# Optimization experiments

Measured on AMD Instinct MI355X. Metric: run time of the kernel, lower is better.

Reference implementation:

```python
import jax, jax.numpy as jnp
import numpy as np

HID, NL, DSTATE, DCONV, EXPAND = 256, 2, 64, 4, 2
DIN = EXPAND * HID            # 512
NHEADS = DIN // 64            # 8 heads, headdim 64
HEADP = DIN // NHEADS         # 64
CONVDIM = DIN + 2 * DSTATE    # 640
PROJDIM = 2 * DIN + 2 * DSTATE + NHEADS  # 1160
B, T, NB = 2, 192, 62


def _rmsnorm(x, w, eps=1e-6):
    return x * jax.lax.rsqrt(jnp.mean(x * x, -1, keepdims=True) + eps) * w


def _causal_conv(x, w, b):
    # x (B,L,C), depthwise causal conv, w (C,K), b (C,)
    K = w.shape[1]
    L = x.shape[1]
    xp = jnp.pad(x, ((0, 0), (K - 1, 0), (0, 0)))
    y = b
    for k in range(K):
        y = y + xp[:, k:k + L, :] * w[:, k]
    return y


def _ssd(xh, dt, A, Bm, Cm):
    # quadratic (attention-like) form of the Mamba2 selective scan
    # xh (b,l,h,p), dt (b,l,h), A (h,), Bm/Cm (b,l,n)
    cum = jnp.cumsum(dt * A, axis=1)                    # (b,l,h)
    diff = cum[:, :, None, :] - cum[:, None, :, :]      # (b,l,s,h), <=0 for s<=l
    mask = jnp.tril(jnp.ones((xh.shape[1], xh.shape[1]), bool))
    decay = jnp.where(mask[None, :, :, None], jnp.exp(diff), 0.0)
    scores = jnp.einsum('bln,bsn->bls', Cm, Bm)[..., None] * decay * dt[:, None, :, :]
    return jnp.einsum('blsh,bshp->blhp', scores, xh)


def _mamba2(x, Win, Wconv, bconv, dt_bias, A_log, D, gn_w, Wout):
    b, l, _ = x.shape
    zxbcdt = x @ Win                                    # (b,l,PROJDIM)
    z = zxbcdt[..., :DIN]
    xBC = jax.nn.silu(_causal_conv(zxbcdt[..., DIN:DIN + CONVDIM], Wconv, bconv))
    xh = xBC[..., :DIN].reshape(b, l, NHEADS, HEADP)
    Bm = xBC[..., DIN:DIN + DSTATE]
    Cm = xBC[..., DIN + DSTATE:]
    dt = jax.nn.softplus(zxbcdt[..., -NHEADS:] + dt_bias)
    A = -jnp.exp(A_log)
    rev = lambda t: t[:, ::-1]
    y = _ssd(xh, dt, A, Bm, Cm) + rev(_ssd(rev(xh), rev(dt), A, rev(Bm), rev(Cm)))
    y = y + D[None, None, :, None] * xh
    y = _rmsnorm(y.reshape(b, l, DIN) * jax.nn.silu(z), gn_w)
    return y @ Wout


def _forward(x, tp, bp):
    batch, T_, NB_, H_ = x.shape
    for i in range(NL):
        # time axis: sequences of length T over batch*num_bands
        xt = jnp.transpose(x, (0, 2, 1, 3)).reshape(batch * NB_, T_, H_)
        xt = xt + _mamba2(_rmsnorm(xt, tp[0][i]), *(p[i] for p in tp[1:]))
        x = jnp.transpose(xt.reshape(batch, NB_, T_, H_), (0, 2, 1, 3))
        # band axis: sequences of length NB over batch*time
        xb = x.reshape(batch * T_, NB_, H_)
        xb = xb + _mamba2(_rmsnorm(xb, bp[0][i]), *(p[i] for p in bp[1:]))
        x = xb.reshape(batch, T_, NB_, H_)
    return x


def setup_inputs() -> dict:
    key = jax.random.key(0)
    ks = jax.random.split(key, 3)
    inp = {"x": jax.random.normal(ks[0], (B, T, NB, HID), jnp.float32)}
    for i, ax in enumerate(("t", "b")):
        kk = jax.random.split(ks[1 + i], 5)
        inp[ax + "_norm_w"] = jnp.ones((NL, HID), jnp.float32)
        inp[ax + "_Win"] = jax.random.normal(kk[0], (NL, HID, PROJDIM), jnp.float32) * HID ** -0.5
        inp[ax + "_Wconv"] = jax.random.normal(kk[1], (NL, CONVDIM, DCONV), jnp.float32) * DCONV ** -0.5
        inp[ax + "_bconv"] = jnp.zeros((NL, CONVDIM), jnp.float32)
        dt = jnp.exp(jax.random.uniform(kk[2], (NL, NHEADS)) * (np.log(0.1) - np.log(0.001)) + np.log(0.001))
        inp[ax + "_dt_bias"] = jnp.log(jnp.expm1(dt)).astype(jnp.float32)
        inp[ax + "_A_log"] = jnp.log(jax.random.uniform(kk[3], (NL, NHEADS), minval=1.0, maxval=16.0)).astype(jnp.float32)
        inp[ax + "_D"] = jnp.ones((NL, NHEADS), jnp.float32)
        inp[ax + "_gn_w"] = jnp.ones((NL, DIN), jnp.float32)
        inp[ax + "_Wout"] = jax.random.normal(kk[4], (NL, DIN, HID), jnp.float32) * DIN ** -0.5
    return inp


def reference(x, t_norm_w, t_Win, t_Wconv, t_bconv, t_dt_bias, t_A_log, t_D, t_gn_w, t_Wout,
              b_norm_w, b_Win, b_Wconv, b_bconv, b_dt_bias, b_A_log, b_D, b_gn_w, b_Wout):
    tp = (t_norm_w, t_Win, t_Wconv, t_bconv, t_dt_bias, t_A_log, t_D, t_gn_w, t_Wout)
    bp = (b_norm_w, b_Win, b_Wconv, b_bconv, b_dt_bias, b_A_log, b_D, b_gn_w, b_Wout)
    return _forward(x, tp, bp)
```

## Files before the change

kernel.cpp:

```cpp
#include <hip/hip_runtime.h>
#include <hip/hip_bf16.h>


#define MTOK   23808
#define PROJP  1280
#define ZXW    1152

typedef __attribute__((ext_vector_type(8))) short short8v;
typedef __attribute__((ext_vector_type(4))) short short4v;
typedef __attribute__((ext_vector_type(4))) float f32x4;

__device__ __forceinline__ float wave_sum64(float v) {
#pragma unroll
  for (int off = 32; off; off >>= 1) v += __shfl_xor(v, off, 64);
  return v;
}

__device__ __forceinline__ short f2bf(float f) {
  union { float f; unsigned u; } v; v.f = f;
  unsigned r = (v.u + 0x7fffu + ((v.u >> 16) & 1u)) >> 16;
  return (short)r;
}
__device__ __forceinline__ float bf2f(short s) {
  union { unsigned u; float f; } v; v.u = ((unsigned)(unsigned short)s) << 16; return v.f;
}

__device__ __forceinline__ long t_base(int m) {
  int seq = m / 192, tt = m - seq * 192;
  int b = seq / 62, nb = seq - b * 62;
  return ((long)((b * 192 + tt) * 62 + nb)) * 256;
}

__global__ __launch_bounds__(256) void k_wt(const float* __restrict__ tW,
                                            const float* __restrict__ bW,
                                            short* __restrict__ dst, int K, int N, int NP) {
  int z = blockIdx.z;
  const float* src = (z >> 1 ? bW : tW) + (long)(z & 1) * K * N;
  short* d = dst + (long)z * NP * K;
  int idx = blockIdx.x * 256 + threadIdx.x;
  if (idx >= NP * K) return;
  int n = idx / K, k = idx - n * K;
  d[idx] = (n < N) ? f2bf(src[(long)k * N + n]) : (short)0;
}

template <bool TPATH>
__global__ __launch_bounds__(256) void k_rmsnorm_in(const float* __restrict__ xio,
                                                    const float* __restrict__ w,
                                                    short* __restrict__ outb) {
  int m = blockIdx.x * 4 + (threadIdx.x >> 6);
  int lane = threadIdx.x & 63;
  long base = TPATH ? t_base(m) : (long)m * 256;
  float4 v = *(const float4*)(xio + base + lane * 4);
  float ss = v.x * v.x + v.y * v.y + v.z * v.z + v.w * v.w;
  ss = wave_sum64(ss);
  float sc = rsqrtf(ss * (1.f / 256.f) + 1e-6f);
  float4 wv = *(const float4*)(w + lane * 4);
  short4v o;
  o[0] = f2bf(v.x * sc * wv.x); o[1] = f2bf(v.y * sc * wv.y);
  o[2] = f2bf(v.z * sc * wv.z); o[3] = f2bf(v.w * sc * wv.w);
  *(short4v*)(outb + (long)m * 256 + lane * 4) = o;
}

__global__ __launch_bounds__(256) void gemm_in(const short* __restrict__ A,
                                               const short* __restrict__ WT,
                                               short* __restrict__ zxh,
                                               float* __restrict__ dtraw) {
  int bid = blockIdx.y * 10 + blockIdx.x;
  int xcd = bid & 7, idx = bid >> 3;
  const int q = 232, r = 4;
  int wg = (xcd < r ? xcd * (q + 1) : r * (q + 1) + (xcd - r) * q) + idx;
  int bx = wg % 10, by = wg / 10;

  int w = threadIdx.x >> 6, lane = threadIdx.x & 63;
  int m0 = by * 128 + (w >> 1) * 64;
  int n0 = bx * 128 + (w & 1) * 64;
  int lr = lane & 15, lg = lane >> 4;
  f32x4 acc[4][4];
#pragma unroll
  for (int i = 0; i < 4; ++i)
#pragma unroll
    for (int j = 0; j < 4; ++j) acc[i][j] = (f32x4){0.f, 0.f, 0.f, 0.f};
  const short* Ap = A + (long)(m0 + lr) * 256 + lg * 8;
  const short* Bp = WT + (long)(n0 + lr) * 256 + lg * 8;
#pragma unroll 2
  for (int k0 = 0; k0 < 256; k0 += 32) {
    short8v a[4], b[4];
#pragma unroll
    for (int f = 0; f < 4; ++f) {
      a[f] = *(const short8v*)(Ap + (long)f * 16 * 256 + k0);
      b[f] = *(const short8v*)(Bp + (long)f * 16 * 256 + k0);
    }
#pragma unroll
    for (int i = 0; i < 4; ++i)
#pragma unroll
      for (int j = 0; j < 4; ++j)
        acc[i][j] = __builtin_amdgcn_mfma_f32_16x16x32_bf16(a[i], b[j], acc[i][j], 0, 0, 0);
  }
  if (n0 < ZXW) {
#pragma unroll
    for (int i = 0; i < 4; ++i)
#pragma unroll
      for (int j = 0; j < 4; ++j)
#pragma unroll
        for (int rr = 0; rr < 4; ++rr) {
          int m = m0 + i * 16 + lg * 4 + rr;
          zxh[(long)m * ZXW + n0 + j * 16 + lr] = f2bf(acc[i][j][rr]);
        }
  } else if (n0 == ZXW && lr < 8) {
#pragma unroll
    for (int i = 0; i < 4; ++i)
#pragma unroll
      for (int rr = 0; rr < 4; ++rr) {
        int m = m0 + i * 16 + lg * 4 + rr;
        dtraw[(long)m * 8 + lr] = acc[i][0][rr];
      }
  }
}

template <int EPI>
__global__ __launch_bounds__(256) void gemm_mfma(const short* __restrict__ A,
                                                 const short* __restrict__ WT,
                                                 float* __restrict__ C,
                                                 int K, int ldc) {
  int w = threadIdx.x >> 6, lane = threadIdx.x & 63;
  int m0 = blockIdx.y * 128 + (w >> 1) * 64;
  int n0 = blockIdx.x * 128 + (w & 1) * 64;
  int lr = lane & 15, lg = lane >> 4;
  f32x4 acc[4][4];
#pragma unroll
  for (int i = 0; i < 4; ++i)
#pragma unroll
    for (int j = 0; j < 4; ++j) acc[i][j] = (f32x4){0.f, 0.f, 0.f, 0.f};
  const short* Ap = A + (long)(m0 + lr) * K + lg * 8;
  const short* Bp = WT + (long)(n0 + lr) * K + lg * 8;
#pragma unroll 2
  for (int k0 = 0; k0 < K; k0 += 32) {
    short8v a[4], b[4];
#pragma unroll
    for (int f = 0; f < 4; ++f) {
      a[f] = *(const short8v*)(Ap + (long)f * 16 * K + k0);
      b[f] = *(const short8v*)(Bp + (long)f * 16 * K + k0);
    }
#pragma unroll
    for (int i = 0; i < 4; ++i)
#pragma unroll
      for (int j = 0; j < 4; ++j)
        acc[i][j] = __builtin_amdgcn_mfma_f32_16x16x32_bf16(a[i], b[j], acc[i][j], 0, 0, 0);
  }
#pragma unroll
  for (int i = 0; i < 4; ++i)
#pragma unroll
    for (int j = 0; j < 4; ++j)
#pragma unroll
      for (int rr = 0; rr < 4; ++rr) {
        int m = m0 + i * 16 + lg * 4 + rr;
        int n = n0 + j * 16 + lr;
        long base = (EPI == 1) ? t_base(m) : (long)m * 256;
        C[base + n] += acc[i][j][rr];
      }
}

__global__ __launch_bounds__(256) void k_conv(const short* __restrict__ zin,
                                              const float* __restrict__ Wc,
                                              const float* __restrict__ bc,
                                              short* __restrict__ xBC, int L) {
  int idx = blockIdx.x * 256 + threadIdx.x;
  if (idx >= MTOK * 80) return;
  int m = idx / 80, c8 = (idx - m * 80) << 3;
  int tpos = m % L;
  float wv[8][4];
#pragma unroll
  for (int e = 0; e < 8; ++e) {
    float4 we = *(const float4*)(Wc + (c8 + e) * 4);
    wv[e][0] = we.x; wv[e][1] = we.y; wv[e][2] = we.z; wv[e][3] = we.w;
  }
  float acc[8];
  float4 b0 = *(const float4*)(bc + c8);
  float4 b1 = *(const float4*)(bc + c8 + 4);
  acc[0] = b0.x; acc[1] = b0.y; acc[2] = b0.z; acc[3] = b0.w;
  acc[4] = b1.x; acc[5] = b1.y; acc[6] = b1.z; acc[7] = b1.w;
  const short* base = zin + (long)m * ZXW + 512 + c8;
#pragma unroll
  for (int k = 0; k < 4; ++k) {
    int tt = tpos - 3 + k;
    if (tt >= 0) {
      short8v v = *(const short8v*)(base + (long)(k - 3) * ZXW);
#pragma unroll
      for (int e = 0; e < 8; ++e) acc[e] += wv[e][k] * bf2f(v[e]);
    }
  }
  short8v o;
#pragma unroll
  for (int e = 0; e < 8; ++e) o[e] = f2bf(acc[e] / (1.f + __expf(-acc[e])));
  *(short8v*)(xBC + (long)m * 640 + c8) = o;
}

__global__ __launch_bounds__(256) void k_scan(const float* __restrict__ dtraw,
                                              const float* __restrict__ dtbias,
                                              const float* __restrict__ A_log,
                                              float* __restrict__ dtb,
                                              float* __restrict__ cumb,
                                              int nseq, int L) {
  int wid = blockIdx.x * 4 + (threadIdx.x >> 6);
  if (wid >= nseq * 8) return;
  int seq = wid >> 3, h = wid & 7, lane = threadIdx.x & 63;
  float Ah = -__expf(A_log[h]);
  float bias = dtbias[h];
  float run = 0.f;
  for (int t0 = 0; t0 < L; t0 += 64) {
    int tt = t0 + lane;
    float d = 0.f;
    if (tt < L) {
      float v = dtraw[((long)seq * L + tt) * 8 + h] + bias;
      d = (v > 20.f) ? v : log1pf(__expf(v));
    }
    float s = d * Ah;
#pragma unroll
    for (int off = 1; off < 64; off <<= 1) {
      float o = __shfl_up(s, off, 64);
      if (lane >= off) s += o;
    }
    if (tt < L) {
      long m = (long)seq * L + tt;
      dtb[m * 8 + h] = d;
      cumb[m * 8 + h] = run + s;
    }
    run += __shfl(s, 63, 64);
  }
}

template <int L>
__global__ __launch_bounds__(256) void k_xt(const short* __restrict__ xbc,
                                            short* __restrict__ xT) {
  constexpr int LP = (L + 63) & ~63;
  int seq = blockIdx.x, h = blockIdx.y, st = blockIdx.z;
  __shared__ short tile[64][72];
  int t = threadIdx.x;
  for (int e = t; e < 512; e += 256) {
    int s = e >> 3, p8 = (e & 7) * 8;
    int sg = st * 64 + s;
    union { short8v v; short a[8]; } u;
    if (sg < L) u.v = *(const short8v*)(xbc + ((long)seq * L + sg) * 640 + h * 64 + p8);
    else {
#pragma unroll
      for (int j = 0; j < 8; ++j) u.a[j] = 0;
    }
    *(short8v*)&tile[s][p8] = u.v;
  }
  __syncthreads();
  for (int e = t; e < 512; e += 256) {
    int p = e >> 3, s8 = (e & 7) * 8;
    union { short8v v; short a[8]; } u;
#pragma unroll
    for (int j = 0; j < 8; ++j) u.a[j] = tile[s8 + j][p];
    *(short8v*)(xT + ((long)(seq * 8 + h) * 64 + p) * LP + st * 64 + s8) = u.v;
  }
}

template <int L, int NCH>
__global__ __launch_bounds__(256) void k_ssd4(const short* __restrict__ xbc,
                                              const short* __restrict__ xT,
                                              const float* __restrict__ dtb,
                                              const float* __restrict__ cumb,
                                              const float* __restrict__ A_log,
                                              short* __restrict__ y) {
  constexpr int LP = (L + 63) & ~63;
  constexpr bool FULL = (L % 64) == 0;
  int hg = blockIdx.x, lt = blockIdx.y, seq = blockIdx.z;
  int tid = threadIdx.x, w = tid >> 6, lane = tid & 63;
  int lr = lane & 15, lg = lane >> 4;
  int h = hg * 4 + w;
  int l0 = lt * 64;

  __shared__ float s_cb[64 * 64];
  __shared__ float s_cums[64][8];
  __shared__ float s_dts[64][8];

  float Ah = -__expf(A_log[h]);

  float cl[4], cpl[4];
#pragma unroll
  for (int i = 0; i < 4; ++i) {
    int lgl = l0 + i * 16 + lr;
    int lc = FULL ? lgl : (lgl < L ? lgl : L - 1);
    long m = (long)seq * L + lc;
    float cv = cumb[m * 8 + h];
    cl[i] = cv; cpl[i] = cv - dtb[m * 8 + h] * Ah;
  }

  f32x4 yacc[4][4];
#pragma unroll
  for (int i = 0; i < 4; ++i)
#pragma unroll
    for (int j = 0; j < 4; ++j) yacc[i][j] = (f32x4){0.f, 0.f, 0.f, 0.f};

  int crow = l0 + w * 16 + lr;
  if (!FULL) crow = crow < L ? crow : L - 1;
  const short* Cp = xbc + ((long)seq * L + crow) * 640 + 576 + lg * 8;

  for (int c = 0; c < NCH; ++c) {
    int c64 = c * 64;

    if (tid < 128) {
      int rr = tid & 63;
      int sg = c64 + rr;
      int sc = FULL ? sg : (sg < L ? sg : L - 1);
      const float* src = (tid < 64 ? cumb : dtb) + ((long)seq * L + sc) * 8;
      float4 v0 = *(const float4*)(src);
      float4 v1 = *(const float4*)(src + 4);
      float* dstp = (tid < 64 ? &s_cums[rr][0] : &s_dts[rr][0]);
      *(float4*)dstp = v0;
      *(float4*)(dstp + 4) = v1;
    }

    f32x4 cb4[4];
#pragma unroll
    for (int j = 0; j < 4; ++j) cb4[j] = (f32x4){0.f, 0.f, 0.f, 0.f};
#pragma unroll
    for (int ks = 0; ks < 2; ++ks) {
      short8v a = *(const short8v*)(Cp + ks * 32);
#pragma unroll
      for (int j = 0; j < 4; ++j) {
        int srow = c64 + j * 16 + lr;
        if (!FULL) srow = srow < L ? srow : L - 1;
        short8v b = *(const short8v*)(xbc + ((long)seq * L + srow) * 640 + 512 + lg * 8 + ks * 32);
        cb4[j] = __builtin_amdgcn_mfma_f32_16x16x32_bf16(a, b, cb4[j], 0, 0, 0);
      }
    }
#pragma unroll
    for (int j = 0; j < 4; ++j)
#pragma unroll
      for (int rr = 0; rr < 4; ++rr) {
        int lloc = w * 16 + lg * 4 + rr;
        int sloc = j * 16 + lr;
        s_cb[lloc * 64 + (sloc ^ ((lloc & 7) << 2))] = cb4[j][rr];
      }

    short8v bx[2][4];
#pragma unroll
    for (int ks = 0; ks < 2; ++ks)
#pragma unroll
      for (int j = 0; j < 4; ++j)
        bx[ks][j] = *(const short8v*)(xT + ((long)(seq * 8 + h) * 64 + j * 16 + lr) * LP +
                                      c64 + ks * 32 + lg * 8);

    __syncthreads();

#pragma unroll
    for (int ks = 0; ks < 2; ++ks) {
      int sbase = ks * 32 + lg * 8;
      float cs[8], cps[8], dss[8];
#pragma unroll
      for (int e = 0; e < 8; ++e) {
        int sl = sbase + e;
        float cv = s_cums[sl][h];
        float dv = s_dts[sl][h];
        cs[e] = cv; cps[e] = cv - dv * Ah; dss[e] = dv;
      }
#pragma unroll
      for (int i = 0; i < 4; ++i) {
        int R = i * 16 + lr;
        int lgl = l0 + R;
        int sw = (R & 7) << 2;
        int c0 = sbase ^ sw;
        const float* cbrow = &s_cb[R * 64];
        f32x4 lo = *(const f32x4*)(cbrow + c0);
        f32x4 hi = *(const f32x4*)(cbrow + (c0 ^ 4));
        short8v a;
#pragma unroll
        for (int e = 0; e < 8; ++e) {
          int sgl = c64 + sbase + e;
          float cbv = (e < 4) ? lo[e & 3] : hi[e & 3];
          float wgt = 0.f;
          if (sgl <= lgl) wgt += __expf(cl[i] - cs[e]);
          if (sgl >= lgl) wgt += __expf(cps[e] - cpl[i]);
          if (!FULL && (lgl >= L || sgl >= L)) wgt = 0.f;
          a[e] = f2bf(cbv * wgt * dss[e]);
        }
#pragma unroll
        for (int j = 0; j < 4; ++j)
          yacc[i][j] = __builtin_amdgcn_mfma_f32_16x16x32_bf16(a, bx[ks][j], yacc[i][j], 0, 0, 0);
      }
    }
    if (c + 1 < NCH) __syncthreads();
  }

#pragma unroll
  for (int i = 0; i < 4; ++i)
#pragma unroll
    for (int rr = 0; rr < 4; ++rr) {
      int lgl = l0 + i * 16 + lg * 4 + rr;
      if (FULL || lgl < L) {
        short* yp = y + ((long)seq * L + lgl) * 512 + h * 64 + lr;
#pragma unroll
        for (int j = 0; j < 4; ++j) yp[j * 16] = f2bf(yacc[i][j][rr]);
      }
    }
}

__global__ __launch_bounds__(256) void k_gate2(const short* __restrict__ y,
                                               const short* __restrict__ zxh,
                                               const short* __restrict__ xbc,
                                               const float* __restrict__ Dp,
                                               const float* __restrict__ gnw,
                                               short* __restrict__ ybh) {
  int m = blockIdx.x * 4 + (threadIdx.x >> 6);
  int lane = threadIdx.x & 63;
  int d0 = lane * 8;
  short8v yv = *(const short8v*)(y + (long)m * 512 + d0);
  short8v xv = *(const short8v*)(xbc + (long)m * 640 + d0);
  short8v zv = *(const short8v*)(zxh + (long)m * ZXW + d0);
  float Dh = Dp[lane >> 3];
  float g[8];
  float ss = 0.f;
#pragma unroll
  for (int i = 0; i < 8; ++i) {
    float zi = bf2f(zv[i]);
    g[i] = (bf2f(yv[i]) + Dh * bf2f(xv[i])) * zi / (1.f + __expf(-zi));
    ss += g[i] * g[i];
  }
  ss = wave_sum64(ss);
  float scl = rsqrtf(ss * (1.f / 512.f) + 1e-6f);
  short8v o;
#pragma unroll
  for (int i = 0; i < 8; ++i) o[i] = f2bf(g[i] * scl * gnw[d0 + i]);
  *(short8v*)(ybh + (long)m * 512 + d0) = o;
}

extern "C" void kernel_launch(void* const* d_in, const int* in_sizes, int n_in,
                              void* d_out, int out_size, void* d_ws, size_t ws_size,
                              hipStream_t stream) {
  (void)in_sizes; (void)n_in; (void)out_size; (void)ws_size;
  const float* x = (const float*)d_in[0];
  float* out = (float*)d_out;
  const long M = MTOK;

  char* p = (char*)d_ws;
  short* zxh = (short*)p;    p += (size_t)M * ZXW * 2;
  float* dtraw = (float*)p;  p += (size_t)M * 8 * 4;
  short* bufn = (short*)p;   p += (size_t)M * 256 * 2;
  short* xbc = (short*)p;    p += (size_t)M * 640 * 2 + 4096;
  float* dtb = (float*)p;    p += (size_t)M * 8 * 4;
  float* cumb = (float*)p;   p += (size_t)M * 8 * 4;
  short* ybuf = (short*)p;   p += (size_t)M * 512 * 2;
  short* xT = (short*)p;     p += (size_t)12582912 * 2;
  short* ybh = (short*)p;    p += (size_t)M * 512 * 2;
  short* WinT = (short*)p;   p += (size_t)4 * PROJP * 256 * 2;
  short* WoutT = (short*)p;  p += (size_t)4 * 256 * 512 * 2;

  k_wt<<<dim3((PROJP * 256 + 255) / 256, 1, 4), 256, 0, stream>>>(
      (const float*)d_in[2], (const float*)d_in[11], WinT, 256, 1160, PROJP);
  k_wt<<<dim3((256 * 512 + 255) / 256, 1, 4), 256, 0, stream>>>(
      (const float*)d_in[9], (const float*)d_in[18], WoutT, 512, 256, 256);

  hipMemcpyAsync(out, x, (size_t)M * 256 * sizeof(float), hipMemcpyDeviceToDevice, stream);

  for (int layer = 0; layer < 2; ++layer) {
    for (int path = 0; path < 2; ++path) {
      const float* const* P = (const float* const*)(d_in + 1 + path * 9);
      const float* nw = P[0] + layer * 256;
      const float* Wc = P[2] + layer * 640 * 4;
      const float* bc = P[3] + layer * 640;
      const float* dtbias = P[4] + layer * 8;
      const float* Alog = P[5] + layer * 8;
      const float* Dp = P[6] + layer * 8;
      const float* gnw = P[7] + layer * 512;
      const short* WinTp = WinT + (long)(path * 2 + layer) * PROJP * 256;
      const short* WoutTp = WoutT + (long)(path * 2 + layer) * 256 * 512;
      int L = (path == 0) ? 192 : 62;
      int nseq = (path == 0) ? 124 : 384;

      if (path == 0) k_rmsnorm_in<true><<<MTOK / 4, 256, 0, stream>>>(out, nw, bufn);
      else           k_rmsnorm_in<false><<<MTOK / 4, 256, 0, stream>>>(out, nw, bufn);

      gemm_in<<<dim3(10, MTOK / 128), 256, 0, stream>>>(bufn, WinTp, zxh, dtraw);

      k_conv<<<(MTOK * 80 + 255) / 256, 256, 0, stream>>>(zxh, Wc, bc, xbc, L);
      k_scan<<<(nseq * 8 + 3) / 4, 256, 0, stream>>>(dtraw, dtbias, Alog, dtb, cumb, nseq, L);

      if (path == 0) k_xt<192><<<dim3(nseq, 8, 3), 256, 0, stream>>>(xbc, xT);
      else           k_xt<62><<<dim3(nseq, 8, 1), 256, 0, stream>>>(xbc, xT);

      if (path == 0) k_ssd4<192, 3><<<dim3(2, 3, nseq), 256, 0, stream>>>(xbc, xT, dtb, cumb, Alog, ybuf);
      else           k_ssd4<62, 1><<<dim3(2, 1, nseq), 256, 0, stream>>>(xbc, xT, dtb, cumb, Alog, ybuf);

      k_gate2<<<MTOK / 4, 256, 0, stream>>>(ybuf, zxh, xbc, Dp, gnw, ybh);

      if (path == 0) gemm_mfma<1><<<dim3(2, MTOK / 128), 256, 0, stream>>>(ybh, WoutTp, out, 512, 0);
      else           gemm_mfma<2><<<dim3(2, MTOK / 128), 256, 0, stream>>>(ybh, WoutTp, out, 512, 0);
    }
  }
}
```

Before: 1.060 ms.

## Use single-wave 64x64 GEMM blocks with register prefetch and LDS-staged stores

Both the input and output projection GEMMs now run one 64-thread wave per 64x64 output tile instead of a four-wave 128x128 block. This raises the block count so more CUs are busy. The K loop double-buffers the A/B fragment loads in registers so the next slice is fetched while the current MFMAs run. Epilogues go through a padded shared-memory tile so global stores, and the read-add-write of the residual, are coalesced 16-byte vectors instead of scattered scalars. Blocks are remapped across XCDs for L2 locality. The smaller tiles give less operand reuse per block, and the output GEMM now launches with grid.x=4 instead of 2, covering columns 0-255 in 64-wide tiles.

```diff
diff --git a/kernel.cpp b/kernel.cpp
--- a/kernel.cpp
+++ b/kernel.cpp
@@ -29,6 +29,12 @@
   int seq = m / 192, tt = m - seq * 192;
   int b = seq / 62, nb = seq - b * 62;
   return ((long)((b * 192 + tt) * 62 + nb)) * 256;
+}
+
+__device__ __forceinline__ int xcd_swz(int bid, int nwg) {
+  int q = nwg >> 3, r = nwg & 7;
+  int xcd = bid & 7, idx = bid >> 3;
+  return (xcd < r ? xcd * (q + 1) : r * (q + 1) + (xcd - r) * q) + idx;
 }
 
 __global__ __launch_bounds__(256) void k_wt(const float* __restrict__ tW,
@@ -61,103 +67,138 @@
   *(short4v*)(outb + (long)m * 256 + lane * 4) = o;
 }
 
-__global__ __launch_bounds__(256) void gemm_in(const short* __restrict__ A,
+__global__ __launch_bounds__(64) void gemm_in2(const short* __restrict__ A,
                                                const short* __restrict__ WT,
                                                short* __restrict__ zxh,
                                                float* __restrict__ dtraw) {
-  int bid = blockIdx.y * 10 + blockIdx.x;
-  int xcd = bid & 7, idx = bid >> 3;
-  const int q = 232, r = 4;
-  int wg = (xcd < r ? xcd * (q + 1) : r * (q + 1) + (xcd - r) * q) + idx;
-  int bx = wg % 10, by = wg / 10;
-
-  int w = threadIdx.x >> 6, lane = threadIdx.x & 63;
-  int m0 = by * 128 + (w >> 1) * 64;
-  int n0 = bx * 128 + (w & 1) * 64;
+  __shared__ short s_t[64][72];
+  int bid = blockIdx.y * 19 + blockIdx.x;
+  int wg = xcd_swz(bid, 19 * 372);
+  int bx = wg % 19, by = wg / 19;
+  int m0 = by * 64, n0 = bx * 64;
+  int lane = threadIdx.x;
   int lr = lane & 15, lg = lane >> 4;
+
   f32x4 acc[4][4];
 #pragma unroll
   for (int i = 0; i < 4; ++i)
 #pragma unroll
     for (int j = 0; j < 4; ++j) acc[i][j] = (f32x4){0.f, 0.f, 0.f, 0.f};
+
   const short* Ap = A + (long)(m0 + lr) * 256 + lg * 8;
   const short* Bp = WT + (long)(n0 + lr) * 256 + lg * 8;
-#pragma unroll 2
-  for (int k0 = 0; k0 < 256; k0 += 32) {
-    short8v a[4], b[4];
-#pragma unroll
-    for (int f = 0; f < 4; ++f) {
-      a[f] = *(const short8v*)(Ap + (long)f * 16 * 256 + k0);
-      b[f] = *(const short8v*)(Bp + (long)f * 16 * 256 + k0);
+
+  short8v a[2][4], b[2][4];
+#pragma unroll
+  for (int f = 0; f < 4; ++f) {
+    a[0][f] = *(const short8v*)(Ap + f * 16 * 256);
+    b[0][f] = *(const short8v*)(Bp + f * 16 * 256);
+  }
+#pragma unroll
+  for (int k = 0; k < 8; ++k) {
+    const int cur = k & 1, nxt = cur ^ 1;
+    if (k < 7) {
+#pragma unroll
+      for (int f = 0; f < 4; ++f) {
+        a[nxt][f] = *(const short8v*)(Ap + f * 16 * 256 + (k + 1) * 32);
+        b[nxt][f] = *(const short8v*)(Bp + f * 16 * 256 + (k + 1) * 32);
+      }
     }
 #pragma unroll
     for (int i = 0; i < 4; ++i)
 #pragma unroll
       for (int j = 0; j < 4; ++j)
-        acc[i][j] = __builtin_amdgcn_mfma_f32_16x16x32_bf16(a[i], b[j], acc[i][j], 0, 0, 0);
-  }
+        acc[i][j] = __builtin_amdgcn_mfma_f32_16x16x32_bf16(a[cur][i], b[cur][j], acc[i][j], 0, 0, 0);
+  }
+
   if (n0 < ZXW) {
 #pragma unroll
     for (int i = 0; i < 4; ++i)
 #pragma unroll
       for (int j = 0; j < 4; ++j)
 #pragma unroll
-        for (int rr = 0; rr < 4; ++rr) {
-          int m = m0 + i * 16 + lg * 4 + rr;
-          zxh[(long)m * ZXW + n0 + j * 16 + lr] = f2bf(acc[i][j][rr]);
-        }
-  } else if (n0 == ZXW && lr < 8) {
+        for (int rr = 0; rr < 4; ++rr)
+          s_t[i * 16 + lg * 4 + rr][j * 16 + lr] = f2bf(acc[i][j][rr]);
+    __syncthreads();
+#pragma unroll
+    for (int rb = 0; rb < 8; ++rb) {
+      int row = rb * 8 + (lane >> 3);
+      short8v v = *(const short8v*)&s_t[row][(lane & 7) * 8];
+      *(short8v*)(zxh + (long)(m0 + row) * ZXW + n0 + (lane & 7) * 8) = v;
+    }
+  } else {
+    if (lr < 8) {
+#pragma unroll
+      for (int i = 0; i < 4; ++i)
+#pragma unroll
+        for (int rr = 0; rr < 4; ++rr)
+          dtraw[(long)(m0 + i * 16 + lg * 4 + rr) * 8 + lr] = acc[i][0][rr];
+    }
+  }
+}
+
+template <int EPI>
+__global__ __launch_bounds__(64) void gemm_out2(const short* __restrict__ A,
+                                                const short* __restrict__ WT,
+                                                float* __restrict__ C) {
+  __shared__ float s_t[64][68];
+  int bid = blockIdx.y * 4 + blockIdx.x;
+  int wg = xcd_swz(bid, 4 * 372);
+  int bx = wg & 3, by = wg >> 2;
+  int m0 = by * 64, n0 = bx * 64;
+  int lane = threadIdx.x;
+  int lr = lane & 15, lg = lane >> 4;
+
+  f32x4 acc[4][4];
+#pragma unroll
+  for (int i = 0; i < 4; ++i)
+#pragma unroll
+    for (int j = 0; j < 4; ++j) acc[i][j] = (f32x4){0.f, 0.f, 0.f, 0.f};
+
+  const short* Ap = A + (long)(m0 + lr) * 512 + lg * 8;
+  const short* Bp = WT + (long)(n0 + lr) * 512 + lg * 8;
+
+  short8v a[2][4], b[2][4];
+#pragma unroll
+  for (int f = 0; f < 4; ++f) {
+    a[0][f] = *(const short8v*)(Ap + f * 16 * 512);
+    b[0][f] = *(const short8v*)(Bp + f * 16 * 512);
+  }
+#pragma unroll
+  for (int k = 0; k < 16; ++k) {
+    const int cur = k & 1, nxt = cur ^ 1;
+    if (k < 15) {
+#pragma unroll
+      for (int f = 0; f < 4; ++f) {
+        a[nxt][f] = *(const short8v*)(Ap + f * 16 * 512 + (k + 1) * 32);
+        b[nxt][f] = *(const short8v*)(Bp + f * 16 * 512 + (k + 1) * 32);
+      }
+    }
 #pragma unroll
     for (int i = 0; i < 4; ++i)
 #pragma unroll
-      for (int rr = 0; rr < 4; ++rr) {
-        int m = m0 + i * 16 + lg * 4 + rr;
-        dtraw[(long)m * 8 + lr] = acc[i][0][rr];
-      }
-  }
-}
-
-template <int EPI>
-__global__ __launch_bounds__(256) void gemm_mfma(const short* __restrict__ A,
-                                                 const short* __restrict__ WT,
-                                                 float* __restrict__ C,
-                                                 int K, int ldc) {
-  int w = threadIdx.x >> 6, lane = threadIdx.x & 63;
-  int m0 = blockIdx.y * 128 + (w >> 1) * 64;
-  int n0 = blockIdx.x * 128 + (w & 1) * 64;
-  int lr = lane & 15, lg = lane >> 4;
-  f32x4 acc[4][4];
+      for (int j = 0; j < 4; ++j)
+        acc[i][j] = __builtin_amdgcn_mfma_f32_16x16x32_bf16(a[cur][i], b[cur][j], acc[i][j], 0, 0, 0);
+  }
+
 #pragma unroll
   for (int i = 0; i < 4; ++i)
 #pragma unroll
-    for (int j = 0; j < 4; ++j) acc[i][j] = (f32x4){0.f, 0.f, 0.f, 0.f};
-  const short* Ap = A + (long)(m0 + lr) * K + lg * 8;
-  const short* Bp = WT + (long)(n0 + lr) * K + lg * 8;
-#pragma unroll 2
-  for (int k0 = 0; k0 < K; k0 += 32) {
-    short8v a[4], b[4];
-#pragma unroll
-    for (int f = 0; f < 4; ++f) {
-      a[f] = *(const short8v*)(Ap + (long)f * 16 * K + k0);
-      b[f] = *(const short8v*)(Bp + (long)f * 16 * K + k0);
-    }
-#pragma unroll
-    for (int i = 0; i < 4; ++i)
-#pragma unroll
-      for (int j = 0; j < 4; ++j)
-        acc[i][j] = __builtin_amdgcn_mfma_f32_16x16x32_bf16(a[i], b[j], acc[i][j], 0, 0, 0);
-  }
-#pragma unroll
-  for (int i = 0; i < 4; ++i)
-#pragma unroll
     for (int j = 0; j < 4; ++j)
 #pragma unroll
-      for (int rr = 0; rr < 4; ++rr) {
-        int m = m0 + i * 16 + lg * 4 + rr;
-        int n = n0 + j * 16 + lr;
-        long base = (EPI == 1) ? t_base(m) : (long)m * 256;
-        C[base + n] += acc[i][j][rr];
-      }
+      for (int rr = 0; rr < 4; ++rr)
+        s_t[i * 16 + lg * 4 + rr][j * 16 + lr] = acc[i][j][rr];
+  __syncthreads();
+#pragma unroll
+  for (int rb = 0; rb < 16; ++rb) {
+    int row = rb * 4 + (lane >> 4);
+    f32x4 v = *(const f32x4*)&s_t[row][lr * 4];
+    int m = m0 + row;
+    long base = (EPI == 1) ? t_base(m) : (long)m * 256;
+    float* cp = C + base + n0 + lr * 4;
+    float4 old = *(const float4*)cp;
+    *(float4*)cp = make_float4(old.x + v[0], old.y + v[1], old.z + v[2], old.w + v[3]);
+  }
 }
 
 __global__ __launch_bounds__(256) void k_conv(const short* __restrict__ zin,
@@ -473,7 +514,7 @@
       if (path == 0) k_rmsnorm_in<true><<<MTOK / 4, 256, 0, stream>>>(out, nw, bufn);
       else           k_rmsnorm_in<false><<<MTOK / 4, 256, 0, stream>>>(out, nw, bufn);
 
-      gemm_in<<<dim3(10, MTOK / 128), 256, 0, stream>>>(bufn, WinTp, zxh, dtraw);
+      gemm_in2<<<dim3(19, MTOK / 64), 64, 0, stream>>>(bufn, WinTp, zxh, dtraw);
 
       k_conv<<<(MTOK * 80 + 255) / 256, 256, 0, stream>>>(zxh, Wc, bc, xbc, L);
       k_scan<<<(nseq * 8 + 3) / 4, 256, 0, stream>>>(dtraw, dtbias, Alog, dtb, cumb, nseq, L);
@@ -486,8 +527,8 @@
 
       k_gate2<<<MTOK / 4, 256, 0, stream>>>(ybuf, zxh, xbc, Dp, gnw, ybh);
 
-      if (path == 0) gemm_mfma<1><<<dim3(2, MTOK / 128), 256, 0, stream>>>(ybh, WoutTp, out, 512, 0);
-      else           gemm_mfma<2><<<dim3(2, MTOK / 128), 256, 0, stream>>>(ybh, WoutTp, out, 512, 0);
-    }
-  }
-}
+      if (path == 0) gemm_out2<1><<<dim3(4, MTOK / 64), 64, 0, stream>>>(ybh, WoutTp, out);
+      else           gemm_out2<2><<<dim3(4, MTOK / 64), 64, 0, stream>>>(ybh, WoutTp, out);
+    }
+  }
+}
```

Measured after the change: 1.008 ms. 4.9% less time.
